# Performance work log

Hardware: AMD Instinct MI355X
Metric: run time of the kernel (lower is better)

## Reference

```python
import jax, jax.numpy as jnp
import numpy as np

B, S, D, H = 2, 2048, 1024, 16
HD = D // H  # head_dim = 64


def setup_inputs() -> dict:
    key = jax.random.key(0)
    ks = jax.random.split(key, 9)
    s_in = 1.0 / np.sqrt(D)
    inp = {
        "hidden_state": jax.random.normal(ks[0], (B, S, D), dtype=jnp.float32),
        # per-head projections, stacked: [H, D, HD]
        "Wq": jax.random.uniform(ks[1], (H, D, HD), jnp.float32, -s_in, s_in),
        "bq": jax.random.uniform(ks[2], (H, HD), jnp.float32, -s_in, s_in),
        "Wk": jax.random.uniform(ks[3], (H, D, HD), jnp.float32, -s_in, s_in),
        "bk": jax.random.uniform(ks[4], (H, HD), jnp.float32, -s_in, s_in),
        "Wv": jax.random.uniform(ks[5], (H, D, HD), jnp.float32, -s_in, s_in),
        "bv": jax.random.uniform(ks[6], (H, HD), jnp.float32, -s_in, s_in),
        # output linear: [D, D]
        "Wo": jax.random.uniform(ks[7], (D, D), jnp.float32, -s_in, s_in),
        "bo": jax.random.uniform(ks[8], (D,), jnp.float32, -s_in, s_in),
    }
    return inp


def reference(hidden_state, Wq, bq, Wk, bk, Wv, bv, Wo, bo):
    # fused per-head projections: [B, H, S, HD]
    q = jnp.einsum("bsd,hde->bhse", hidden_state, Wq) + bq[None, :, None, :]
    k = jnp.einsum("bsd,hde->bhse", hidden_state, Wk) + bk[None, :, None, :]
    v = jnp.einsum("bsd,hde->bhse", hidden_state, Wv) + bv[None, :, None, :]
    scale = 1.0 / jnp.sqrt(jnp.float32(HD))
    scores = jnp.einsum("bhse,bhte->bhst", q, k) * scale  # [B, H, S, S]
    weights = jax.nn.softmax(scores, axis=-1)
    ctx = jnp.einsum("bhst,bhte->bhse", weights, v)       # [B, H, S, HD]
    # concat heads along last dim -> [B, S, D]
    ctx = jnp.transpose(ctx, (0, 2, 1, 3)).reshape(B, S, D)
    return ctx @ Wo + bo
```

## Files before the change

### kernel.cpp

```cpp
#include <hip/hip_runtime.h>
#include <hip/hip_bf16.h>
#include <math.h>

#define BB 2
#define SS 2048
#define DD 1024
#define HH 16
#define HD 64

typedef __attribute__((ext_vector_type(8))) _Float16 f16x8;
typedef __attribute__((ext_vector_type(2))) __fp16 fp16x2;
typedef __attribute__((ext_vector_type(8))) unsigned short u16x8;
typedef __attribute__((ext_vector_type(4))) float f32x4;
typedef __attribute__((ext_vector_type(4))) unsigned short u16x4;

__device__ __forceinline__ unsigned short hbits(_Float16 h) {
    union { _Float16 h; unsigned short s; } u; u.h = h; return u.s;
}

__device__ __forceinline__ int swz(int row, int grp) {
    return (row << 6) + (((grp) ^ (row & 7)) << 3);
}

__device__ __forceinline__ float fexp2(float x) {
#if __has_builtin(__builtin_amdgcn_exp2f)
    return __builtin_amdgcn_exp2f(x);
#else
    return exp2f(x);
#endif
}

__device__ __forceinline__ u16x4 pack4(float p0, float p1, float p2, float p3) {
#if __has_builtin(__builtin_amdgcn_cvt_pkrtz)
    union { fp16x2 h[2]; u16x4 u; } pu;
    pu.h[0] = __builtin_amdgcn_cvt_pkrtz(p0, p1);
    pu.h[1] = __builtin_amdgcn_cvt_pkrtz(p2, p3);
    return pu.u;
#else
    u16x4 r;
    r[0] = hbits((_Float16)p0); r[1] = hbits((_Float16)p1);
    r[2] = hbits((_Float16)p2); r[3] = hbits((_Float16)p3);
    return r;
#endif
}

__device__ __forceinline__ void gload_lds16(const unsigned short* g, unsigned short* l) {
#if __has_builtin(__builtin_amdgcn_global_load_lds)
    auto gp = (const __attribute__((address_space(1))) unsigned int*)(uintptr_t)g;
    auto lp = (__attribute__((address_space(3))) unsigned int*)(uintptr_t)l;
    __builtin_amdgcn_global_load_lds(gp, lp, 16, 0, 0);
#else
    *(u16x8*)(l + (threadIdx.x & 63) * 8) = *(const u16x8*)g;
#endif
}

__device__ __forceinline__ void wait4_barrier() {
    asm volatile("s_waitcnt vmcnt(4) lgkmcnt(0)\n\ts_barrier" ::: "memory");
}
__device__ __forceinline__ void wait8_barrier() {
    asm volatile("s_waitcnt vmcnt(8) lgkmcnt(0)\n\ts_barrier" ::: "memory");
}
__device__ __forceinline__ void wait0_barrier() {
    asm volatile("s_waitcnt vmcnt(0) lgkmcnt(0)\n\ts_barrier" ::: "memory");
}

__global__ __launch_bounds__(256) void prep_convert(
    const float* __restrict__ X,
    const float* __restrict__ Wq, const float* __restrict__ Wk,
    const float* __restrict__ Wv, const float* __restrict__ Wo,
    unsigned short* __restrict__ Xh, unsigned short* __restrict__ WT)
{
    __shared__ __align__(16) unsigned short LT[64 * 68];
    const int bid = blockIdx.x;
    const int tid = threadIdx.x;

    if (bid < 2048) {
        const int base = bid * 2048 + tid * 8;
        float4 a = *(const float4*)&X[base];
        float4 b = *(const float4*)&X[base + 4];
        u16x8 o;
        o[0] = hbits((_Float16)a.x); o[1] = hbits((_Float16)a.y);
        o[2] = hbits((_Float16)a.z); o[3] = hbits((_Float16)a.w);
        o[4] = hbits((_Float16)b.x); o[5] = hbits((_Float16)b.y);
        o[6] = hbits((_Float16)b.z); o[7] = hbits((_Float16)b.w);
        *(u16x8*)&Xh[base] = o;
        return;
    }

    const int t = bid - 2048;
    const float* src;
    size_t stride;
    int outRow0, kcol0;
    if (t < 768) {
        const int nt = t >> 4, ktile = t & 15;
        const int sel = nt >> 4, hh = nt & 15;
        const float* Ws = (sel == 0) ? Wq : ((sel == 1) ? Wk : Wv);
        src = Ws + (size_t)hh * (DD * HD) + (size_t)ktile * 64 * HD;
        stride = HD;
        outRow0 = nt * 64;
        kcol0 = ktile * 64;
    } else {
        const int tt = t - 768;
        const int nt = tt & 15, ktile = tt >> 4;
        src = Wo + (size_t)ktile * 64 * DD + nt * 64;
        stride = DD;
        outRow0 = 3072 + nt * 64;
        kcol0 = ktile * 64;
    }

    const int e = tid & 63, dq = tid >> 6;
#pragma unroll
    for (int p = 0; p < 16; p++) {
        const int dl = p * 4 + dq;
        LT[e * 68 + dl] = hbits((_Float16)src[(size_t)dl * stride + e]);
    }
    __syncthreads();
    const int eo = tid >> 2, d16 = (tid & 3) * 16;
#pragma unroll
    for (int j = 0; j < 4; j++) {
        *(ushort4*)&WT[(size_t)(outRow0 + eo) * DD + kcol0 + d16 + j * 4] =
            *(const ushort4*)&LT[eo * 68 + d16 + j * 4];
    }
}

#define GBM 128
#define GBN 128
#define GBK 64
#define NKT (DD / GBK)
#define QBK 32
#define QNKT (DD / QBK)

__global__ __launch_bounds__(256) void qkv_gemm(
    const unsigned short* __restrict__ Xh, const unsigned short* __restrict__ WT,
    const float* __restrict__ bq, const float* __restrict__ bk,
    const float* __restrict__ bv,
    unsigned short* __restrict__ qh, unsigned short* __restrict__ kh,
    unsigned short* __restrict__ vTs, unsigned int* __restrict__ kc2)
{
    __shared__ __align__(16) unsigned short As[3][8 * 512];
    __shared__ __align__(16) unsigned short Bs[3][8 * 512];

    const int tid = threadIdx.x;
    const int m0 = blockIdx.y * GBM;
    const int n0 = blockIdx.x * GBN;
    const int lane = tid & 63;
    const int w = tid >> 6;
    const int wm = w & 1, wn = w >> 1;
    const int l15 = lane & 15, quad = lane >> 4;

    int g_off[2];
#pragma unroll
    for (int p = 0; p < 2; p++) {
        const int c = p * 4 + w;
        g_off[p] = (c * 16 + l15) * DD + quad * 8;
    }

    f32x4 acc[4][4];
#pragma unroll
    for (int i = 0; i < 4; i++)
#pragma unroll
        for (int j = 0; j < 4; j++) acc[i][j] = (f32x4){0.f, 0.f, 0.f, 0.f};

    const unsigned short* Abase = Xh + (size_t)m0 * DD;
    const unsigned short* Bbase = WT + (size_t)n0 * DD;

#pragma unroll
    for (int p = 0; p < 2; p++) {
        gload_lds16(Abase + g_off[p], &As[0][(p * 4 + w) * 512]);
        gload_lds16(Bbase + g_off[p], &Bs[0][(p * 4 + w) * 512]);
    }
#pragma unroll
    for (int p = 0; p < 2; p++) {
        gload_lds16(Abase + g_off[p] + QBK, &As[1][(p * 4 + w) * 512]);
        gload_lds16(Bbase + g_off[p] + QBK, &Bs[1][(p * 4 + w) * 512]);
    }
    wait0_barrier();

    int cur = 0, pre = 2;
    for (int t = 0; t < QNKT; t++) {
        if (t + 2 < QNKT) {
            const int kt2 = (t + 2) * QBK;
#pragma unroll
            for (int p = 0; p < 2; p++) {
                gload_lds16(Abase + g_off[p] + kt2, &As[pre][(p * 4 + w) * 512]);
                gload_lds16(Bbase + g_off[p] + kt2, &Bs[pre][(p * 4 + w) * 512]);
            }
        }
        f16x8 af[4], bf[4];
#pragma unroll
        for (int i = 0; i < 4; i++) {
            af[i] = *(const f16x8*)&As[cur][(wm * 4 + i) * 512 + lane * 8];
            bf[i] = *(const f16x8*)&Bs[cur][(wn * 4 + i) * 512 + lane * 8];
        }
#pragma unroll
        for (int ns = 0; ns < 4; ns++)
#pragma unroll
            for (int ms = 0; ms < 4; ms++)
                acc[ms][ns] = __builtin_amdgcn_mfma_f32_16x16x32_f16(
                    af[ms], bf[ns], acc[ms][ns], 0, 0, 0);
        if (t < QNKT - 2)       wait4_barrier();
        else if (t == QNKT - 2) wait0_barrier();
        cur = (cur == 2) ? 0 : cur + 1;
        pre = (pre == 2) ? 0 : pre + 1;
    }

    const int sel = n0 >> 10;
    const int hw = ((n0 + wn * 64) >> 6) & 15;
    const int bblk = m0 >> 11;
    const float* bias = (sel == 0) ? bq : ((sel == 1) ? bk : bv);
    const size_t bh_base = ((size_t)bblk * HH + hw) * SS * HD;
    float wmx = 0.0f;
#pragma unroll
    for (int ms = 0; ms < 4; ms++) {
#pragma unroll
        for (int rr = 0; rr < 4; rr++) {
            const int m = m0 + wm * 64 + ms * 16 + quad * 4 + rr;
            const int s = m & (SS - 1);
            const int s63 = s & 63;
            float v2 = 0.0f;
#pragma unroll
            for (int ns = 0; ns < 4; ns++) {
                const int e = ns * 16 + l15;
                const float val = acc[ms][ns][rr] + bias[hw * HD + e];
                if (sel == 0) {
                    qh[bh_base + (size_t)s * HD + e] = hbits((_Float16)val);
                } else if (sel == 1) {
                    v2 = fmaf(val, val, v2);
                    const size_t kofs = bh_base + (size_t)(s >> 6) * 4096
                                      + swz(s63, e >> 3) + (e & 7);
                    kh[kofs] = hbits((_Float16)val);
                } else {
                    const size_t vofs = bh_base + (size_t)(s >> 6) * 4096
                                      + swz(e, s63 >> 3) + (s63 & 7);
                    vTs[vofs] = hbits((_Float16)val);
                }
            }
            if (sel == 1) {
                v2 += __shfl_xor(v2, 1);
                v2 += __shfl_xor(v2, 2);
                v2 += __shfl_xor(v2, 4);
                v2 += __shfl_xor(v2, 8);
                wmx = fmaxf(wmx, v2);
            }
        }
    }
    if (sel == 1) {
        wmx = fmaxf(wmx, __shfl_xor(wmx, 16));
        wmx = fmaxf(wmx, __shfl_xor(wmx, 32));
        if (lane == 0)
            atomicMax(&kc2[bblk * HH + hw], __float_as_uint(wmx));
    }
}

__global__ __launch_bounds__(256) void out_gemm(
    const unsigned short* __restrict__ Ctxh, const unsigned short* __restrict__ WoT,
    const float* __restrict__ bo, float* __restrict__ out)
{
    __shared__ __align__(16) unsigned short As[3][16 * 512];
    __shared__ __align__(16) unsigned short Bs[3][16 * 512];

    const int tid = threadIdx.x;
    const int m0 = blockIdx.y * GBM;
    const int n0 = blockIdx.x * GBN;
    const int lane = tid & 63;
    const int w = tid >> 6;
    const int wm = w & 1, wn = w >> 1;
    const int l15 = lane & 15, quad = lane >> 4;

    int g_off[4];
#pragma unroll
    for (int p = 0; p < 4; p++) {
        const int c = p * 4 + w;
        g_off[p] = ((c >> 1) * 16 + (lane & 15)) * DD + (c & 1) * 32 + (lane >> 4) * 8;
    }

    f32x4 acc[4][4];
#pragma unroll
    for (int i = 0; i < 4; i++)
#pragma unroll
        for (int j = 0; j < 4; j++) acc[i][j] = (f32x4){0.f, 0.f, 0.f, 0.f};

    const unsigned short* Abase = Ctxh + (size_t)m0 * DD;
    const unsigned short* Bbase = WoT + (size_t)n0 * DD;

#pragma unroll
    for (int p = 0; p < 4; p++) {
        gload_lds16(Abase + g_off[p], &As[0][(p * 4 + w) * 512]);
        gload_lds16(Bbase + g_off[p], &Bs[0][(p * 4 + w) * 512]);
    }
#pragma unroll
    for (int p = 0; p < 4; p++) {
        gload_lds16(Abase + g_off[p] + GBK, &As[1][(p * 4 + w) * 512]);
        gload_lds16(Bbase + g_off[p] + GBK, &Bs[1][(p * 4 + w) * 512]);
    }
    wait0_barrier();

    int cur = 0, pre = 2;
    for (int it = 0; it < NKT; it++) {
        if (it + 2 < NKT) {
            const int kt2 = (it + 2) * GBK;
#pragma unroll
            for (int p = 0; p < 4; p++) {
                gload_lds16(Abase + g_off[p] + kt2, &As[pre][(p * 4 + w) * 512]);
                gload_lds16(Bbase + g_off[p] + kt2, &Bs[pre][(p * 4 + w) * 512]);
            }
        }
#pragma unroll
        for (int ks = 0; ks < 2; ks++) {
            f16x8 af[4], bf[4];
#pragma unroll
            for (int i = 0; i < 4; i++) {
                af[i] = *(const f16x8*)&As[cur][((wm * 4 + i) * 2 + ks) * 512 + lane * 8];
                bf[i] = *(const f16x8*)&Bs[cur][((wn * 4 + i) * 2 + ks) * 512 + lane * 8];
            }
#pragma unroll
            for (int ns = 0; ns < 4; ns++)
#pragma unroll
                for (int ms = 0; ms < 4; ms++)
                    acc[ms][ns] = __builtin_amdgcn_mfma_f32_16x16x32_f16(
                        af[ms], bf[ns], acc[ms][ns], 0, 0, 0);
        }
        if (it < NKT - 2)       wait8_barrier();
        else if (it == NKT - 2) wait0_barrier();
        cur = (cur == 2) ? 0 : cur + 1;
        pre = (pre == 2) ? 0 : pre + 1;
    }

#pragma unroll
    for (int ms = 0; ms < 4; ms++) {
#pragma unroll
        for (int rr = 0; rr < 4; rr++) {
            const size_t m = (size_t)(m0 + wm * 64 + ms * 16 + quad * 4 + rr);
#pragma unroll
            for (int ns = 0; ns < 4; ns++) {
                const int n = n0 + wn * 64 + ns * 16 + l15;
                out[m * DD + n] = acc[ms][ns][rr] + bo[n];
            }
        }
    }
}

#define TQB 128
#define TKB 64
#define NT (SS / TKB)
#define C1 0.1803368801111204f

__global__ __launch_bounds__(256) void attn_mfma(
    const unsigned short* __restrict__ qh, const unsigned short* __restrict__ kh,
    const unsigned short* __restrict__ vTs, const unsigned int* __restrict__ kc2,
    unsigned short* __restrict__ ctxh)
{
    __shared__ __align__(16) unsigned short KL [3][TKB * 64];
    __shared__ __align__(16) unsigned short VtL[3][HD * 64];
    __shared__ __align__(16) unsigned short PsL[4][32 * 64];

    const int tid  = threadIdx.x;
    const int lane = tid & 63;
    const int w    = tid >> 6;
    const int l15  = lane & 15;
    const int quad = lane >> 4;
    const int bh   = blockIdx.y;
    const int q0   = blockIdx.x * TQB;

    const float kfac = sqrtf(__uint_as_float(kc2[bh])) * 1.01f * C1;

    f16x8 qf[2][2];
    float M2[2];
#pragma unroll
    for (int msub = 0; msub < 2; msub++) {
        const unsigned short* qrow =
            qh + ((size_t)bh * SS + q0 + w * 32 + msub * 16 + l15) * HD;
        float nq2 = 0.0f;
#pragma unroll
        for (int dstep = 0; dstep < 2; dstep++) {
            qf[msub][dstep] = *(const f16x8*)&qrow[dstep * 32 + quad * 8];
#pragma unroll
            for (int j = 0; j < 8; j++) {
                const float x = (float)qf[msub][dstep][j];
                nq2 = fmaf(x, x, nq2);
            }
        }
        nq2 += __shfl_xor(nq2, 16);
        nq2 += __shfl_xor(nq2, 32);
        M2[msub] = sqrtf(nq2) * kfac;
    }

    f16x8 ones;
#pragma unroll
    for (int j = 0; j < 8; j++) ones[j] = (_Float16)1.0f;

    f32x4 o[2][4], lones[2];
#pragma unroll
    for (int ms = 0; ms < 2; ms++) {
        lones[ms] = (f32x4){0.f, 0.f, 0.f, 0.f};
#pragma unroll
        for (int e = 0; e < 4; e++) o[ms][e] = (f32x4){0.f, 0.f, 0.f, 0.f};
    }

    const unsigned short* kb0 = kh  + (size_t)bh * SS * HD;
    const unsigned short* vb0 = vTs + (size_t)bh * SS * HD;

    gload_lds16(kb0 + tid * 8,        &KL [0][w * 512]);
    gload_lds16(kb0 + 2048 + tid * 8, &KL [0][2048 + w * 512]);
    gload_lds16(vb0 + tid * 8,        &VtL[0][w * 512]);
    gload_lds16(vb0 + 2048 + tid * 8, &VtL[0][2048 + w * 512]);
    gload_lds16(kb0 + 4096 + tid * 8, &KL [1][w * 512]);
    gload_lds16(kb0 + 6144 + tid * 8, &KL [1][2048 + w * 512]);
    gload_lds16(vb0 + 4096 + tid * 8, &VtL[1][w * 512]);
    gload_lds16(vb0 + 6144 + tid * 8, &VtL[1][2048 + w * 512]);
    wait0_barrier();

    int cur = 0, pre = 2;
    for (int t = 0; t < NT; t++) {
        if (t + 2 < NT) {
            const unsigned short* kb = kb0 + (size_t)(t + 2) * 4096;
            const unsigned short* vb = vb0 + (size_t)(t + 2) * 4096;
            gload_lds16(kb + tid * 8,        &KL [pre][w * 512]);
            gload_lds16(kb + 2048 + tid * 8, &KL [pre][2048 + w * 512]);
            gload_lds16(vb + tid * 8,        &VtL[pre][w * 512]);
            gload_lds16(vb + 2048 + tid * 8, &VtL[pre][2048 + w * 512]);
        }

        f32x4 sc[2][4];
#pragma unroll
        for (int ksub = 0; ksub < 4; ksub++) {
            const int row = ksub * 16 + l15;
            f16x8 k0 = *(const f16x8*)&KL[cur][swz(row, quad)];
            f16x8 k1 = *(const f16x8*)&KL[cur][swz(row, 4 + quad)];
#pragma unroll
            for (int msub = 0; msub < 2; msub++) {
                f32x4 a = (f32x4){0.f, 0.f, 0.f, 0.f};
                a = __builtin_amdgcn_mfma_f32_16x16x32_f16(k0, qf[msub][0], a, 0, 0, 0);
                a = __builtin_amdgcn_mfma_f32_16x16x32_f16(k1, qf[msub][1], a, 0, 0, 0);
                sc[msub][ksub] = a;
            }
        }

#pragma unroll
        for (int msub = 0; msub < 2; msub++) {
            const int prow = msub * 16 + l15;
#pragma unroll
            for (int ksub = 0; ksub < 4; ksub++) {
                const float p0 = fexp2(fmaf(sc[msub][ksub][0], C1, -M2[msub]));
                const float p1 = fexp2(fmaf(sc[msub][ksub][1], C1, -M2[msub]));
                const float p2 = fexp2(fmaf(sc[msub][ksub][2], C1, -M2[msub]));
                const float p3 = fexp2(fmaf(sc[msub][ksub][3], C1, -M2[msub]));
                *(u16x4*)&PsL[w][swz(prow, ksub * 2 + (quad >> 1)) + (quad & 1) * 4] =
                    pack4(p0, p1, p2, p3);
            }
        }

#pragma unroll
        for (int kj = 0; kj < 2; kj++) {
            f16x8 pa[2];
#pragma unroll
            for (int msub = 0; msub < 2; msub++)
                pa[msub] = *(const f16x8*)&PsL[w][swz(msub * 16 + l15, kj * 4 + quad)];
            lones[0] = __builtin_amdgcn_mfma_f32_16x16x32_f16(pa[0], ones, lones[0], 0, 0, 0);
            lones[1] = __builtin_amdgcn_mfma_f32_16x16x32_f16(pa[1], ones, lones[1], 0, 0, 0);
#pragma unroll
            for (int esub = 0; esub < 4; esub++) {
                f16x8 vr = *(const f16x8*)&VtL[cur][swz(esub * 16 + l15, kj * 4 + quad)];
                o[0][esub] = __builtin_amdgcn_mfma_f32_16x16x32_f16(pa[0], vr, o[0][esub], 0, 0, 0);
                o[1][esub] = __builtin_amdgcn_mfma_f32_16x16x32_f16(pa[1], vr, o[1][esub], 0, 0, 0);
            }
        }

        if (t < NT - 2)       wait4_barrier();
        else if (t == NT - 2) wait0_barrier();
        cur = (cur == 2) ? 0 : cur + 1;
        pre = (pre == 2) ? 0 : pre + 1;
    }

    const int b = bh >> 4;
    const int h = bh & 15;
#pragma unroll
    for (int msub = 0; msub < 2; msub++) {
#pragma unroll
        for (int rr = 0; rr < 4; rr++) {
            const float linv = 1.0f / lones[msub][rr];
            const int row = q0 + w * 32 + msub * 16 + quad * 4 + rr;
#pragma unroll
            for (int esub = 0; esub < 4; esub++) {
                ctxh[((size_t)b * SS + row) * DD + h * HD + esub * 16 + l15] =
                    hbits((_Float16)(o[msub][esub][rr] * linv));
            }
        }
    }
}

extern "C" void kernel_launch(void* const* d_in, const int* in_sizes, int n_in,
                              void* d_out, int out_size, void* d_ws, size_t ws_size,
                              hipStream_t stream) {
    const float* X  = (const float*)d_in[0];
    const float* Wq = (const float*)d_in[1];
    const float* bq = (const float*)d_in[2];
    const float* Wk = (const float*)d_in[3];
    const float* bk = (const float*)d_in[4];
    const float* Wv = (const float*)d_in[5];
    const float* bv = (const float*)d_in[6];
    const float* Wo = (const float*)d_in[7];
    const float* bo = (const float*)d_in[8];
    float* out = (float*)d_out;

    const size_t NB2 = (size_t)4096 * 1024 * 2;
    unsigned char* w8 = (unsigned char*)d_ws;
    unsigned short* Xh   = (unsigned short*)(w8);
    unsigned short* WT   = (unsigned short*)(w8 + NB2);
    unsigned short* qh   = (unsigned short*)(w8 + 2 * NB2);
    unsigned short* kh   = (unsigned short*)(w8 + 3 * NB2);
    unsigned short* vTs  = (unsigned short*)(w8 + 4 * NB2);
    unsigned short* ctxh = (unsigned short*)(w8 + 5 * NB2);
    unsigned int*   kc2  = (unsigned int*)(w8 + 6 * NB2);
    unsigned short* WoT  = WT + (size_t)3072 * 1024;

    (void)hipMemsetAsync(kc2, 0, BB * HH * sizeof(unsigned int), stream);

    prep_convert<<<dim3(3072), 256, 0, stream>>>(X, Wq, Wk, Wv, Wo, Xh, WT);

    qkv_gemm<<<dim3(3072 / GBN, 4096 / GBM), 256, 0, stream>>>(
        Xh, WT, bq, bk, bv, qh, kh, vTs, kc2);

    attn_mfma<<<dim3(SS / TQB, BB * HH), 256, 0, stream>>>(qh, kh, vTs, kc2, ctxh);

    out_gemm<<<dim3(1024 / GBN, 4096 / GBM), 256, 0, stream>>>(ctxh, WoT, bo, out);
}
```

Measured before the change: 220.5 us.

## Swizzle block order, rotate K start, shrink out_gemm N tile, add setprio

```diff
diff --git a/kernel.cpp b/kernel.cpp
--- a/kernel.cpp
+++ b/kernel.cpp
@@ -57,8 +57,8 @@
 __device__ __forceinline__ void wait4_barrier() {
     asm volatile("s_waitcnt vmcnt(4) lgkmcnt(0)\n\ts_barrier" ::: "memory");
 }
-__device__ __forceinline__ void wait8_barrier() {
-    asm volatile("s_waitcnt vmcnt(8) lgkmcnt(0)\n\ts_barrier" ::: "memory");
+__device__ __forceinline__ void wait6_barrier() {
+    asm volatile("s_waitcnt vmcnt(6) lgkmcnt(0)\n\ts_barrier" ::: "memory");
 }
 __device__ __forceinline__ void wait0_barrier() {
     asm volatile("s_waitcnt vmcnt(0) lgkmcnt(0)\n\ts_barrier" ::: "memory");
@@ -141,12 +141,16 @@
     __shared__ __align__(16) unsigned short Bs[3][8 * 512];
 
     const int tid = threadIdx.x;
-    const int m0 = blockIdx.y * GBM;
-    const int n0 = blockIdx.x * GBN;
+    const int f  = blockIdx.y * 24 + blockIdx.x;
+    const int fs = (f & 7) * 96 + (f >> 3);
+    const int bx = fs % 24, by = fs / 24;
+    const int m0 = by * GBM;
+    const int n0 = bx * GBN;
     const int lane = tid & 63;
     const int w = tid >> 6;
     const int wm = w & 1, wn = w >> 1;
     const int l15 = lane & 15, quad = lane >> 4;
+    const int kstart = (fs * 7) & (QNKT - 1);
 
     int g_off[2];
 #pragma unroll
@@ -164,22 +168,26 @@
     const unsigned short* Abase = Xh + (size_t)m0 * DD;
     const unsigned short* Bbase = WT + (size_t)n0 * DD;
 
-#pragma unroll
-    for (int p = 0; p < 2; p++) {
-        gload_lds16(Abase + g_off[p], &As[0][(p * 4 + w) * 512]);
-        gload_lds16(Bbase + g_off[p], &Bs[0][(p * 4 + w) * 512]);
-    }
-#pragma unroll
-    for (int p = 0; p < 2; p++) {
-        gload_lds16(Abase + g_off[p] + QBK, &As[1][(p * 4 + w) * 512]);
-        gload_lds16(Bbase + g_off[p] + QBK, &Bs[1][(p * 4 + w) * 512]);
+    {
+        const int k0 = kstart * QBK;
+        const int k1 = ((kstart + 1) & (QNKT - 1)) * QBK;
+#pragma unroll
+        for (int p = 0; p < 2; p++) {
+            gload_lds16(Abase + g_off[p] + k0, &As[0][(p * 4 + w) * 512]);
+            gload_lds16(Bbase + g_off[p] + k0, &Bs[0][(p * 4 + w) * 512]);
+        }
+#pragma unroll
+        for (int p = 0; p < 2; p++) {
+            gload_lds16(Abase + g_off[p] + k1, &As[1][(p * 4 + w) * 512]);
+            gload_lds16(Bbase + g_off[p] + k1, &Bs[1][(p * 4 + w) * 512]);
+        }
     }
     wait0_barrier();
 
     int cur = 0, pre = 2;
     for (int t = 0; t < QNKT; t++) {
         if (t + 2 < QNKT) {
-            const int kt2 = (t + 2) * QBK;
+            const int kt2 = ((kstart + t + 2) & (QNKT - 1)) * QBK;
 #pragma unroll
             for (int p = 0; p < 2; p++) {
                 gload_lds16(Abase + g_off[p] + kt2, &As[pre][(p * 4 + w) * 512]);
@@ -257,70 +265,82 @@
     const float* __restrict__ bo, float* __restrict__ out)
 {
     __shared__ __align__(16) unsigned short As[3][16 * 512];
-    __shared__ __align__(16) unsigned short Bs[3][16 * 512];
+    __shared__ __align__(16) unsigned short Bs[3][8 * 512];
 
     const int tid = threadIdx.x;
-    const int m0 = blockIdx.y * GBM;
-    const int n0 = blockIdx.x * GBN;
+    const int f  = blockIdx.y * 16 + blockIdx.x;
+    const int fs = (f & 7) * 64 + (f >> 3);
+    const int bx = fs % 16, by = fs / 16;
+    const int m0 = by * 128;
+    const int n0 = bx * 64;
     const int lane = tid & 63;
     const int w = tid >> 6;
     const int wm = w & 1, wn = w >> 1;
     const int l15 = lane & 15, quad = lane >> 4;
+    const int kstart = (fs * 5) & (NKT - 1);
 
     int g_off[4];
 #pragma unroll
     for (int p = 0; p < 4; p++) {
         const int c = p * 4 + w;
-        g_off[p] = ((c >> 1) * 16 + (lane & 15)) * DD + (c & 1) * 32 + (lane >> 4) * 8;
-    }
-
-    f32x4 acc[4][4];
+        g_off[p] = ((c >> 1) * 16 + l15) * DD + (c & 1) * 32 + quad * 8;
+    }
+
+    f32x4 acc[4][2];
 #pragma unroll
     for (int i = 0; i < 4; i++)
 #pragma unroll
-        for (int j = 0; j < 4; j++) acc[i][j] = (f32x4){0.f, 0.f, 0.f, 0.f};
+        for (int j = 0; j < 2; j++) acc[i][j] = (f32x4){0.f, 0.f, 0.f, 0.f};
 
     const unsigned short* Abase = Ctxh + (size_t)m0 * DD;
     const unsigned short* Bbase = WoT + (size_t)n0 * DD;
 
-#pragma unroll
-    for (int p = 0; p < 4; p++) {
-        gload_lds16(Abase + g_off[p], &As[0][(p * 4 + w) * 512]);
-        gload_lds16(Bbase + g_off[p], &Bs[0][(p * 4 + w) * 512]);
-    }
-#pragma unroll
-    for (int p = 0; p < 4; p++) {
-        gload_lds16(Abase + g_off[p] + GBK, &As[1][(p * 4 + w) * 512]);
-        gload_lds16(Bbase + g_off[p] + GBK, &Bs[1][(p * 4 + w) * 512]);
+    {
+        const int k0 = kstart * GBK;
+        const int k1 = ((kstart + 1) & (NKT - 1)) * GBK;
+#pragma unroll
+        for (int p = 0; p < 4; p++)
+            gload_lds16(Abase + g_off[p] + k0, &As[0][(p * 4 + w) * 512]);
+#pragma unroll
+        for (int p = 0; p < 2; p++)
+            gload_lds16(Bbase + g_off[p] + k0, &Bs[0][(p * 4 + w) * 512]);
+#pragma unroll
+        for (int p = 0; p < 4; p++)
+            gload_lds16(Abase + g_off[p] + k1, &As[1][(p * 4 + w) * 512]);
+#pragma unroll
+        for (int p = 0; p < 2; p++)
+            gload_lds16(Bbase + g_off[p] + k1, &Bs[1][(p * 4 + w) * 512]);
     }
     wait0_barrier();
 
     int cur = 0, pre = 2;
     for (int it = 0; it < NKT; it++) {
         if (it + 2 < NKT) {
-            const int kt2 = (it + 2) * GBK;
-#pragma unroll
-            for (int p = 0; p < 4; p++) {
+            const int kt2 = ((kstart + it + 2) & (NKT - 1)) * GBK;
+#pragma unroll
+            for (int p = 0; p < 4; p++)
                 gload_lds16(Abase + g_off[p] + kt2, &As[pre][(p * 4 + w) * 512]);
+#pragma unroll
+            for (int p = 0; p < 2; p++)
                 gload_lds16(Bbase + g_off[p] + kt2, &Bs[pre][(p * 4 + w) * 512]);
-            }
         }
 #pragma unroll
         for (int ks = 0; ks < 2; ks++) {
-            f16x8 af[4], bf[4];
-#pragma unroll
-            for (int i = 0; i < 4; i++) {
+            f16x8 af[4], bf[2];
+#pragma unroll
+            for (int i = 0; i < 4; i++)
                 af[i] = *(const f16x8*)&As[cur][((wm * 4 + i) * 2 + ks) * 512 + lane * 8];
-                bf[i] = *(const f16x8*)&Bs[cur][((wn * 4 + i) * 2 + ks) * 512 + lane * 8];
-            }
-#pragma unroll
-            for (int ns = 0; ns < 4; ns++)
+#pragma unroll
+            for (int j = 0; j < 2; j++)
+                bf[j] = *(const f16x8*)&Bs[cur][((wn * 2 + j) * 2 + ks) * 512 + lane * 8];
+#pragma unroll
+            for (int ns = 0; ns < 2; ns++)
 #pragma unroll
                 for (int ms = 0; ms < 4; ms++)
                     acc[ms][ns] = __builtin_amdgcn_mfma_f32_16x16x32_f16(
                         af[ms], bf[ns], acc[ms][ns], 0, 0, 0);
         }
-        if (it < NKT - 2)       wait8_barrier();
+        if (it < NKT - 2)       wait6_barrier();
         else if (it == NKT - 2) wait0_barrier();
         cur = (cur == 2) ? 0 : cur + 1;
         pre = (pre == 2) ? 0 : pre + 1;
@@ -332,8 +352,8 @@
         for (int rr = 0; rr < 4; rr++) {
             const size_t m = (size_t)(m0 + wm * 64 + ms * 16 + quad * 4 + rr);
 #pragma unroll
-            for (int ns = 0; ns < 4; ns++) {
-                const int n = n0 + wn * 64 + ns * 16 + l15;
+            for (int ns = 0; ns < 2; ns++) {
+                const int n = n0 + wn * 32 + ns * 16 + l15;
                 out[m * DD + n] = acc[ms][ns][rr] + bo[n];
             }
         }
@@ -359,8 +379,11 @@
     const int w    = tid >> 6;
     const int l15  = lane & 15;
     const int quad = lane >> 4;
-    const int bh   = blockIdx.y;
-    const int q0   = blockIdx.x * TQB;
+    const int f  = blockIdx.y * 16 + blockIdx.x;
+    const int fs = (f & 7) * 64 + (f >> 3);
+    const int bh = fs >> 4;
+    const int q0 = (fs & 15) * TQB;
+    const int t0 = (fs * 7) & (NT - 1);
 
     const float kfac = sqrtf(__uint_as_float(kc2[bh])) * 1.01f * C1;
 
@@ -400,21 +423,26 @@
     const unsigned short* kb0 = kh  + (size_t)bh * SS * HD;
     const unsigned short* vb0 = vTs + (size_t)bh * SS * HD;
 
-    gload_lds16(kb0 + tid * 8,        &KL [0][w * 512]);
-    gload_lds16(kb0 + 2048 + tid * 8, &KL [0][2048 + w * 512]);
-    gload_lds16(vb0 + tid * 8,        &VtL[0][w * 512]);
-    gload_lds16(vb0 + 2048 + tid * 8, &VtL[0][2048 + w * 512]);
-    gload_lds16(kb0 + 4096 + tid * 8, &KL [1][w * 512]);
-    gload_lds16(kb0 + 6144 + tid * 8, &KL [1][2048 + w * 512]);
-    gload_lds16(vb0 + 4096 + tid * 8, &VtL[1][w * 512]);
-    gload_lds16(vb0 + 6144 + tid * 8, &VtL[1][2048 + w * 512]);
+    {
+        const size_t u0 = (size_t)t0 * 4096;
+        const size_t u1 = (size_t)((t0 + 1) & (NT - 1)) * 4096;
+        gload_lds16(kb0 + u0 + tid * 8,        &KL [0][w * 512]);
+        gload_lds16(kb0 + u0 + 2048 + tid * 8, &KL [0][2048 + w * 512]);
+        gload_lds16(vb0 + u0 + tid * 8,        &VtL[0][w * 512]);
+        gload_lds16(vb0 + u0 + 2048 + tid * 8, &VtL[0][2048 + w * 512]);
+        gload_lds16(kb0 + u1 + tid * 8,        &KL [1][w * 512]);
+        gload_lds16(kb0 + u1 + 2048 + tid * 8, &KL [1][2048 + w * 512]);
+        gload_lds16(vb0 + u1 + tid * 8,        &VtL[1][w * 512]);
+        gload_lds16(vb0 + u1 + 2048 + tid * 8, &VtL[1][2048 + w * 512]);
+    }
     wait0_barrier();
 
     int cur = 0, pre = 2;
     for (int t = 0; t < NT; t++) {
         if (t + 2 < NT) {
-            const unsigned short* kb = kb0 + (size_t)(t + 2) * 4096;
-            const unsigned short* vb = vb0 + (size_t)(t + 2) * 4096;
+            const size_t u = (size_t)((t0 + t + 2) & (NT - 1)) * 4096;
+            const unsigned short* kb = kb0 + u;
+            const unsigned short* vb = vb0 + u;
             gload_lds16(kb + tid * 8,        &KL [pre][w * 512]);
             gload_lds16(kb + 2048 + tid * 8, &KL [pre][2048 + w * 512]);
             gload_lds16(vb + tid * 8,        &VtL[pre][w * 512]);
@@ -422,6 +450,7 @@
         }
 
         f32x4 sc[2][4];
+        __builtin_amdgcn_s_setprio(1);
 #pragma unroll
         for (int ksub = 0; ksub < 4; ksub++) {
             const int row = ksub * 16 + l15;
@@ -435,6 +464,7 @@
                 sc[msub][ksub] = a;
             }
         }
+        __builtin_amdgcn_s_setprio(0);
 
 #pragma unroll
         for (int msub = 0; msub < 2; msub++) {
@@ -450,6 +480,7 @@
             }
         }
 
+        __builtin_amdgcn_s_setprio(1);
 #pragma unroll
         for (int kj = 0; kj < 2; kj++) {
             f16x8 pa[2];
@@ -465,6 +496,7 @@
                 o[1][esub] = __builtin_amdgcn_mfma_f32_16x16x32_f16(pa[1], vr, o[1][esub], 0, 0, 0);
             }
         }
+        __builtin_amdgcn_s_setprio(0);
 
         if (t < NT - 2)       wait4_barrier();
         else if (t == NT - 2) wait0_barrier();
@@ -523,5 +555,5 @@
 
     attn_mfma<<<dim3(SS / TQB, BB * HH), 256, 0, stream>>>(qh, kh, vTs, kc2, ctxh);
 
-    out_gemm<<<dim3(1024 / GBN, 4096 / GBM), 256, 0, stream>>>(ctxh, WoT, bo, out);
-}
+    out_gemm<<<dim3(1024 / 64, 4096 / 128), 256, 0, stream>>>(ctxh, WoT, bo, out);
+}
```

Result: slower. 225.7 us (+2.3%).
